# Performance work log

Hardware: AMD Instinct MI355X
Metric: run time of the kernel (lower is better)

The kernel has to match this reference:

```python
import jax, jax.numpy as jnp
import numpy as np

B, S, D = 4, 2048, 1024
NEG = -1e10

def setup_inputs() -> dict:
    key = jax.random.key(0)
    ks = jax.random.split(key, 10)
    inv = 1.0 / np.sqrt(D)
    return {
        "Q": jax.random.normal(ks[0], (B, S, D), dtype=jnp.float32),
        "K": jax.random.normal(ks[1], (B, S, D), dtype=jnp.float32),
        "V": jax.random.normal(ks[2], (B, S, D), dtype=jnp.float32),
        "attention_mask": jax.random.randint(ks[3], (B, 1, S), 0, 2, dtype=jnp.int32),
        "Wq": jax.random.uniform(ks[4], (D, D), jnp.float32, -inv, inv),
        "bq": jnp.zeros((D,), jnp.float32),
        "Wk": jax.random.uniform(ks[5], (D, D), jnp.float32, -inv, inv),
        "bk": jnp.zeros((D,), jnp.float32),
        "Wv": jax.random.uniform(ks[6], (D, D), jnp.float32, -inv, inv),
        "bv": jnp.zeros((D,), jnp.float32),
    }

def reference(Q, K, V, attention_mask, Wq, bq, Wk, bk, Wv, bv):
    # QKV projections (dropout is identity in eval mode)
    q = jnp.einsum('bsd,ed->bse', Q, Wq) + bq  # [B,S,D]
    k = jnp.einsum('bsd,ed->bse', K, Wk) + bk
    v = jnp.einsum('bsd,ed->bse', V, Wv) + bv
    scores = jnp.einsum('bqd,bkd->bqk', q, k) / jnp.sqrt(jnp.float32(D))  # [B,S,S]
    scores = jnp.where(attention_mask == 0, jnp.float32(NEG), scores)
    # additive causal mask: upper triangle (diag=1) gets NEG
    causal = jnp.triu(jnp.full((S, S), NEG, dtype=jnp.float32), k=1)
    scores = scores + causal
    attn = jax.nn.softmax(scores, axis=-1)
    return jnp.einsum('bqk,bkd->bqd', attn, v)
```

## Files before the change

kernel.cpp:

```cpp
#include <hip/hip_runtime.h>
#include <hip/hip_bf16.h>

typedef __bf16 bf16x8 __attribute__((ext_vector_type(8)));
typedef float floatx4 __attribute__((ext_vector_type(4)));
typedef unsigned short ushort_t;

__device__ __forceinline__ bf16x8 load8f(const float* p) {
  const float4* q = reinterpret_cast<const float4*>(p);
  float4 x = q[0], y = q[1];
  bf16x8 r;
  r[0] = (__bf16)x.x; r[1] = (__bf16)x.y; r[2] = (__bf16)x.z; r[3] = (__bf16)x.w;
  r[4] = (__bf16)y.x; r[5] = (__bf16)y.y; r[6] = (__bf16)y.z; r[7] = (__bf16)y.w;
  return r;
}

__device__ __forceinline__ void storeC(float* C, long idx, float v) { C[idx] = v; }
__device__ __forceinline__ void storeC(ushort_t* C, long idx, float v) {
  __bf16 b = (__bf16)v;
  C[idx] = __builtin_bit_cast(ushort_t, b);
}

__device__ __forceinline__ void glds16(const ushort_t* g, ushort_t* l) {
  __builtin_amdgcn_global_load_lds(
      (const __attribute__((address_space(1))) void*)g,
      (__attribute__((address_space(3))) void*)l, 16, 0, 0);
}

__device__ __forceinline__ void bar_raw()  { asm volatile("s_barrier" ::: "memory"); }
__device__ __forceinline__ void lgkm0()    { asm volatile("s_waitcnt lgkmcnt(0)" ::: "memory"); }
__device__ __forceinline__ void wait_vm4() { asm volatile("s_waitcnt vmcnt(4)" ::: "memory"); }
__device__ __forceinline__ void wait_vm0() { asm volatile("s_waitcnt vmcnt(0)" ::: "memory"); }

__global__ __launch_bounds__(256) void cvt3m(
    const float* __restrict__ Q, const float* __restrict__ K,
    const float* __restrict__ V, const float* __restrict__ Wq,
    const float* __restrict__ Wk, const float* __restrict__ Wv,
    ushort_t* __restrict__ dstQ, ushort_t* __restrict__ dstW,
    long nq, long nw,
    const int* __restrict__ mask, int* __restrict__ j0, int S, int B)
{
  const int z = blockIdx.y;
  const long bq = nq >> 11;
  long x = blockIdx.x;
  const float* s; ushort_t* d; long n;
  if (x < bq) {
    s = (z == 0) ? Q : ((z == 1) ? K : V);
    d = dstQ + (long)z * nq; n = nq;
  } else {
    x -= bq;
    s = (z == 0) ? Wq : ((z == 1) ? Wk : Wv);
    d = dstW + (long)z * nw; n = nw;
  }
  const long i = ((x * 256) + threadIdx.x) * 8;
  if (i < n) {
    bf16x8 v = load8f(s + i);
    *reinterpret_cast<bf16x8*>(d + i) = v;
  }
  if (z == 0 && (int)blockIdx.x < B) {
    const int b = blockIdx.x;
    const int* m = mask + (long)b * S;
    const int tid = threadIdx.x;
    int best = S;
    for (int j = tid; j < S; j += 256)
      if (m[j] != 0) best = min(best, j);
    #pragma unroll
    for (int off = 32; off; off >>= 1)
      best = min(best, __shfl_xor(best, off));
    __shared__ int red[4];
    if ((tid & 63) == 0) red[tid >> 6] = best;
    __syncthreads();
    if (tid == 0) j0[b] = min(min(red[0], red[1]), min(red[2], red[3]));
  }
}

template<typename TC>
__device__ __forceinline__ void gemm256_core(
    const ushort_t* __restrict__ Apan,
    const ushort_t* __restrict__ Bpan,
    const float* __restrict__ bias, int bias_mode,
    TC* __restrict__ C, int bm, int bn, int N, int K, int G, float alpha)
{
  __shared__ ushort_t Ab[2][2][128 * 64];
  __shared__ ushort_t Bb[2][2][128 * 64];

  const int tid = threadIdx.x;
  const int wv = tid >> 6;
  const int lane = tid & 63;
  const int wr = wv >> 2, wc = wv & 3;
  const int lr = lane & 15, lq = lane >> 4;

  const int q0 = tid << 4;
  const int r0 = q0 >> 7;
  const int c0 = ((q0 & 127) ^ ((r0 & 7) << 4)) >> 1;
  const int lo0 = q0 >> 1;
  const int lo1 = lo0 + 4096;
  const long Kl = K;

  const ushort_t* As0 = Apan + (long)r0 * Kl + c0;
  const ushort_t* Bs0 = Bpan + (long)r0 * Kl + c0;

  auto stA = [&](int t, int h) {
    const ushort_t* s = As0 + (long)(h * 128) * Kl + t * 64;
    ushort_t* d = &Ab[t & 1][h][0];
    glds16(s, d + lo0);
    glds16(s + 64 * Kl, d + lo1);
  };
  auto stB = [&](int t, int h) {
    const ushort_t* s = Bs0 + (long)(h * 128) * Kl + t * 64;
    ushort_t* d = &Bb[t & 1][h][0];
    glds16(s, d + lo0);
    glds16(s + 64 * Kl, d + lo1);
  };

  const int aco0 = ((lq * 16) ^ ((lr & 7) << 4)) >> 1;
  const int aco1 = ((64 + lq * 16) ^ ((lr & 7) << 4)) >> 1;

  floatx4 acc[8][4];
  #pragma unroll
  for (int i = 0; i < 8; ++i)
    #pragma unroll
    for (int j = 0; j < 4; ++j)
      acc[i][j] = (floatx4){0.f, 0.f, 0.f, 0.f};

  bf16x8 a0[4][2], a1[4][2], b0[2][2], b1[2][2];

  auto ldA4 = [&](bf16x8 (&a)[4][2], int buf, int i0) {
    const ushort_t* Ah = &Ab[buf][wr][lr * 64];
    #pragma unroll
    for (int i = 0; i < 4; ++i) {
      a[i][0] = *reinterpret_cast<const bf16x8*>(Ah + (i0 + i) * 1024 + aco0);
      a[i][1] = *reinterpret_cast<const bf16x8*>(Ah + (i0 + i) * 1024 + aco1);
    }
  };
  auto ldB2 = [&](bf16x8 (&b)[2][2], int buf, int j0) {
    const ushort_t* Bh = &Bb[buf][wc >> 1][(wc & 1) * 4096 + lr * 64];
    #pragma unroll
    for (int j = 0; j < 2; ++j) {
      b[j][0] = *reinterpret_cast<const bf16x8*>(Bh + (j0 + j) * 1024 + aco0);
      b[j][1] = *reinterpret_cast<const bf16x8*>(Bh + (j0 + j) * 1024 + aco1);
    }
  };
  auto MM = [&](int I0, bf16x8 (&AF)[4][2], int J0, bf16x8 (&BF)[2][2]) {
    #pragma unroll
    for (int i = 0; i < 4; ++i)
      #pragma unroll
      for (int j = 0; j < 2; ++j) {
        acc[I0 + i][J0 + j] = __builtin_amdgcn_mfma_f32_16x16x32_bf16(
            AF[i][0], BF[j][0], acc[I0 + i][J0 + j], 0, 0, 0);
        acc[I0 + i][J0 + j] = __builtin_amdgcn_mfma_f32_16x16x32_bf16(
            AF[i][1], BF[j][1], acc[I0 + i][J0 + j], 0, 0, 0);
      }
  };

  stB(0, 0); stB(0, 1);
  stA(0, 0); stA(0, 1);
  stB(1, 0); stB(1, 1);
  wait_vm4();
  bar_raw();

  for (int t = 0; t < G; ++t) {
    const int buf = t & 1;
    ldA4(a0, buf, 0);
    ldB2(b0, buf, 0);
    if (t + 1 < G) stA(t + 1, 0);
    bar_raw(); lgkm0();
    __builtin_amdgcn_s_setprio(1);
    MM(0, a0, 0, b0);
    __builtin_amdgcn_s_setprio(0);
    bar_raw();
    ldB2(b1, buf, 2);
    if (t + 1 < G) stA(t + 1, 1);
    bar_raw(); lgkm0();
    __builtin_amdgcn_s_setprio(1);
    MM(0, a0, 2, b1);
    __builtin_amdgcn_s_setprio(0);
    bar_raw();
    ldA4(a1, buf, 4);
    if (t + 2 < G) stB(t + 2, 0);
    bar_raw(); lgkm0();
    __builtin_amdgcn_s_setprio(1);
    MM(4, a1, 0, b0);
    __builtin_amdgcn_s_setprio(0);
    bar_raw();
    if (t + 2 < G) { stB(t + 2, 1); wait_vm4(); }
    else if (t + 1 < G) wait_vm0();
    bar_raw(); lgkm0();
    __builtin_amdgcn_s_setprio(1);
    MM(4, a1, 2, b1);
    __builtin_amdgcn_s_setprio(0);
    bar_raw();
  }

  #pragma unroll
  for (int i = 0; i < 8; ++i) {
    #pragma unroll
    for (int j = 0; j < 4; ++j) {
      const int row0 = bm * 256 + wr * 128 + i * 16 + lq * 4;
      const int col  = bn * 256 + wc * 64 + j * 16 + lr;
      #pragma unroll
      for (int r = 0; r < 4; ++r) {
        float v = acc[i][j][r] * alpha;
        if (bias_mode == 1) v += bias[col];
        else if (bias_mode == 2) v += bias[row0 + r];
        storeC(C, (long)(row0 + r) * N + col, v);
      }
    }
  }
}

__global__ __launch_bounds__(512) void proj8(
    const ushort_t* __restrict__ Qb, const ushort_t* __restrict__ Wqb,
    const float* __restrict__ bq, const float* __restrict__ bk,
    const float* __restrict__ bv,
    ushort_t* __restrict__ qk, ushort_t* __restrict__ vT,
    long NQ, long NW)
{
  const int h = blockIdx.x;
  const int s = (h & 7) * 48 + (h >> 3);
  int bm, bn, N, mode;
  const ushort_t *A, *Bp;
  ushort_t* Cc;
  const float* bias;
  if (s < 256) {
    const int z = s >> 7, r = s & 127;
    bm = r >> 2; bn = r & 3;
    A  = Qb + (long)z * NQ + (long)bm * 256 * 1024;
    Bp = Wqb + (long)z * NW + (long)bn * 256 * 1024;
    Cc = qk + (long)z * NQ;
    bias = z ? bk : bq; mode = 1; N = 1024;
  } else {
    const int u = s - 256, vb = u >> 5, r = u & 31;
    bm = r >> 3; bn = r & 7;
    A  = Wqb + 2 * NW + (long)bm * 256 * 1024;
    Bp = Qb + 2 * NQ + (long)vb * (2048L * 1024) + (long)bn * 256 * 1024;
    Cc = vT + (long)vb * (1024L * 2048);
    bias = bv; mode = 2; N = 2048;
  }
  gemm256_core<ushort_t>(A, Bp, bias, mode, Cc, bm, bn, N, 1024, 16, 1.0f);
}

__global__ __launch_bounds__(512) void scores8(
    const ushort_t* __restrict__ qb, const ushort_t* __restrict__ kb,
    ushort_t* __restrict__ Sc, const int* __restrict__ j0p)
{
  const int h = blockIdx.x;
  const int job = (h & 7) * 32 + (h >> 3);
  const int bz = job >> 6;
  const int s = job & 63;
  int bm, bn;
  if (s < 36) {
    int r = 0;
    while ((r + 1) * (r + 2) / 2 <= s) ++r;
    bm = r; bn = s - r * (r + 1) / 2;
  } else {
    int u = s - 36, r = 0;
    while (u >= 7 - r) { u -= 7 - r; ++r; }
    bm = r; bn = r + 1 + u;
  }
  if (bn > bm && j0p[bz] <= bm * 256) return;
  const long SD = 2048L * 1024;
  gemm256_core<ushort_t>(qb + (long)bz * SD + (long)bm * 256 * 1024,
                         kb + (long)bz * SD + (long)bn * 256 * 1024,
                         nullptr, 0, Sc + (long)bz * 2048 * 2048,
                         bm, bn, 2048, 1024, 16, 0.03125f);
}

__global__ __launch_bounds__(512) void pv8(
    const ushort_t* __restrict__ P, const ushort_t* __restrict__ vT,
    float* __restrict__ out, float* __restrict__ scr,
    const int* __restrict__ j0p)
{
  const int h = blockIdx.x;
  const int job = (h & 7) * 32 + (h >> 3);
  const int bz = job >> 6;
  const int r = job & 63;
  const int bm = r >> 3;
  const int kh = (r >> 2) & 1;
  const int bn = r & 3;

  const int Gf = (j0p[bz] <= bm * 256) ? (bm + 1) * 4 : 32;
  int g0, g1;
  if (Gf > 8) {
    const int half = Gf >> 1;
    g0 = kh ? half : 0;
    g1 = kh ? Gf : half;
  } else {
    if (kh) return;
    g0 = 0; g1 = Gf;
  }

  float* Cc = kh ? (scr + (long)bz * (2048L * 1024))
                 : (out + (long)bz * (2048L * 1024));
  gemm256_core<float>(
      P  + (long)bz * (2048L * 2048) + (long)bm * 256 * 2048 + g0 * 64,
      vT + (long)bz * (1024L * 2048) + (long)bn * 256 * 2048 + g0 * 64,
      nullptr, 0, Cc, bm, bn, 1024, 2048, g1 - g0, 1.0f);
}

__global__ __launch_bounds__(256) void pv_combine(
    float* __restrict__ out, const float* __restrict__ scr,
    const int* __restrict__ j0p)
{
  const long u = (((long)blockIdx.x * 256) + threadIdx.x) * 8;
  const int bz = (int)(u >> 21);
  const long rem = u & ((1L << 21) - 1);
  const int row = (int)(rem >> 10);
  const int bm = row >> 8;
  const int Gf = (j0p[bz] <= bm * 256) ? (bm + 1) * 4 : 32;
  if (Gf <= 8) return;
  float4* o = reinterpret_cast<float4*>(out + u);
  const float4* s = reinterpret_cast<const float4*>(scr + u);
  float4 o0 = o[0], o1 = o[1], s0 = s[0], s1 = s[1];
  o0.x += s0.x; o0.y += s0.y; o0.z += s0.z; o0.w += s0.w;
  o1.x += s1.x; o1.y += s1.y; o1.z += s1.z; o1.w += s1.w;
  o[0] = o0; o[1] = o1;
}

__global__ __launch_bounds__(256) void softmax_causal(
    const ushort_t* __restrict__ Sc, ushort_t* __restrict__ P,
    const int* __restrict__ mask, const int* __restrict__ j0p, int S)
{
  const int i = blockIdx.x, b = blockIdx.y;
  const ushort_t* row = Sc + ((long)b * S + i) * S;
  ushort_t* prow = P + ((long)b * S + i) * S;
  const int* mrow = mask + (long)b * S;
  const int tid = threadIdx.x;
  const int lane = tid & 63, wave = tid >> 6;
  const int j0 = tid * 8;
  __shared__ float red[4];

  const int blk = i >> 8;
  const int jmax = (j0p[b] <= (blk << 8)) ? ((blk + 1) << 8) : S;
  const bool act = (j0 < jmax);

  float vals[8];
  float mymax = -3.4e38f;
  if (act) {
    bf16x8 sv = *reinterpret_cast<const bf16x8*>(row + j0);
    const int4* mp = reinterpret_cast<const int4*>(mrow + j0);
    int4 m0 = mp[0], m1 = mp[1];
    int mk[8] = {m0.x, m0.y, m0.z, m0.w, m1.x, m1.y, m1.z, m1.w};
    #pragma unroll
    for (int u = 0; u < 8; ++u) {
      const int j = j0 + u;
      float v = (float)sv[u];
      if (mk[u] == 0) v = -1e10f;
      if (j > i) v += -1e10f;
      vals[u] = v;
      mymax = fmaxf(mymax, v);
    }
  }
  #pragma unroll
  for (int off = 32; off; off >>= 1)
    mymax = fmaxf(mymax, __shfl_xor(mymax, off));
  if (lane == 0) red[wave] = mymax;
  __syncthreads();
  const float m = fmaxf(fmaxf(red[0], red[1]), fmaxf(red[2], red[3]));
  __syncthreads();

  float sum = 0.f;
  if (act) {
    #pragma unroll
    for (int u = 0; u < 8; ++u) {
      const float e = __expf(vals[u] - m);
      vals[u] = e;
      sum += e;
    }
  }
  #pragma unroll
  for (int off = 32; off; off >>= 1)
    sum += __shfl_xor(sum, off);
  if (lane == 0) red[wave] = sum;
  __syncthreads();
  const float tot = red[0] + red[1] + red[2] + red[3];
  const float inv = 1.0f / tot;

  if (act) {
    bf16x8 pv;
    #pragma unroll
    for (int u = 0; u < 8; ++u) pv[u] = (__bf16)(vals[u] * inv);
    *reinterpret_cast<bf16x8*>(prow + j0) = pv;
  }
}

extern "C" void kernel_launch(void* const* d_in, const int* in_sizes, int n_in,
                              void* d_out, int out_size, void* d_ws, size_t ws_size,
                              hipStream_t stream)
{
  const int B = 4, S = 2048, D = 1024;
  const float* Q  = (const float*)d_in[0];
  const float* K  = (const float*)d_in[1];
  const float* V  = (const float*)d_in[2];
  const int*   am = (const int*)d_in[3];
  const float* Wq = (const float*)d_in[4];
  const float* bq = (const float*)d_in[5];
  const float* Wk = (const float*)d_in[6];
  const float* bk = (const float*)d_in[7];
  const float* Wv = (const float*)d_in[8];
  const float* bv = (const float*)d_in[9];
  float* out = (float*)d_out;

  const long MS = (long)B * S;
  const long NQ = MS * D;
  const long NW = (long)D * D;

  ushort_t* qb = (ushort_t*)d_ws;
  ushort_t* kb = qb + NQ;
  ushort_t* vT = kb + NQ;
  ushort_t* Qb = vT + NQ;
  ushort_t* Wqb = Qb + 3 * NQ;
  int* j0 = (int*)(Wqb + 3 * NW);
  ushort_t* Sc = Qb;
  ushort_t* P  = qb;
  float* scr   = (float*)Qb;

  cvt3m<<<dim3((int)(NQ / 2048 + NW / 2048), 3), dim3(256), 0, stream>>>(
      Q, K, V, Wq, Wk, Wv, Qb, Wqb, NQ, NW, am, j0, S, B);

  proj8<<<dim3(384), dim3(512), 0, stream>>>(Qb, Wqb, bq, bk, bv, qb, vT, NQ, NW);

  scores8<<<dim3(256), dim3(512), 0, stream>>>(qb, kb, Sc, j0);

  softmax_causal<<<dim3(S, B), dim3(256), 0, stream>>>(Sc, P, am, j0, S);

  pv8<<<dim3(256), dim3(512), 0, stream>>>(P, vT, out, scr, j0);
  pv_combine<<<dim3((int)(MS * D / 8 / 256)), dim3(256), 0, stream>>>(out, scr, j0);
}
```

Baseline: 322.5 us.

## Restructure GEMM main loop to one barrier per tile with staged lgkm waits

Replaces the four-phase inner loop, which had a barrier and a full LDS wait around each MFMA quarter, with a single-phase schedule. All global-to-LDS loads for the next tile are issued up front, all LDS fragment reads for the current tile follow, and each MFMA group waits only on its own reads through partial lgkmcnt counts. One vmcnt(0) and one barrier close each iteration. This is meant to cut barrier and wait overhead and overlap LDS reads with MFMA. In exchange the prefetch distance drops from two B tiles ahead to one tile, and the partial lgkmcnt thresholds have to match the exact number of issued LDS reads.

```diff
diff --git a/kernel.cpp b/kernel.cpp
--- a/kernel.cpp
+++ b/kernel.cpp
@@ -27,9 +27,19 @@
 }
 
 __device__ __forceinline__ void bar_raw()  { asm volatile("s_barrier" ::: "memory"); }
-__device__ __forceinline__ void lgkm0()    { asm volatile("s_waitcnt lgkmcnt(0)" ::: "memory"); }
-__device__ __forceinline__ void wait_vm4() { asm volatile("s_waitcnt vmcnt(4)" ::: "memory"); }
 __device__ __forceinline__ void wait_vm0() { asm volatile("s_waitcnt vmcnt(0)" ::: "memory"); }
+__device__ __forceinline__ void wlg12() {
+  asm volatile("s_waitcnt lgkmcnt(12)" ::: "memory");
+  __builtin_amdgcn_sched_barrier(0);
+}
+__device__ __forceinline__ void wlg8() {
+  asm volatile("s_waitcnt lgkmcnt(8)" ::: "memory");
+  __builtin_amdgcn_sched_barrier(0);
+}
+__device__ __forceinline__ void wlg0() {
+  asm volatile("s_waitcnt lgkmcnt(0)" ::: "memory");
+  __builtin_amdgcn_sched_barrier(0);
+}
 
 __global__ __launch_bounds__(256) void cvt3m(
     const float* __restrict__ Q, const float* __restrict__ K,
@@ -152,42 +162,35 @@
       }
   };
 
-  stB(0, 0); stB(0, 1);
-  stA(0, 0); stA(0, 1);
-  stB(1, 0); stB(1, 1);
-  wait_vm4();
+  stA(0, 0); stA(0, 1); stB(0, 0); stB(0, 1);
+  wait_vm0();
   bar_raw();
 
   for (int t = 0; t < G; ++t) {
     const int buf = t & 1;
+    if (t + 1 < G) { stA(t + 1, 0); stA(t + 1, 1); stB(t + 1, 0); stB(t + 1, 1); }
+    __builtin_amdgcn_sched_barrier(0);
     ldA4(a0, buf, 0);
     ldB2(b0, buf, 0);
-    if (t + 1 < G) stA(t + 1, 0);
-    bar_raw(); lgkm0();
+    __builtin_amdgcn_sched_barrier(0);
+    ldB2(b1, buf, 2);
+    __builtin_amdgcn_sched_barrier(0);
+    ldA4(a1, buf, 4);
+    __builtin_amdgcn_sched_barrier(0);
+    wlg12();
     __builtin_amdgcn_s_setprio(1);
     MM(0, a0, 0, b0);
     __builtin_amdgcn_s_setprio(0);
-    bar_raw();
-    ldB2(b1, buf, 2);
-    if (t + 1 < G) stA(t + 1, 1);
-    bar_raw(); lgkm0();
+    wlg8();
     __builtin_amdgcn_s_setprio(1);
     MM(0, a0, 2, b1);
     __builtin_amdgcn_s_setprio(0);
-    bar_raw();
-    ldA4(a1, buf, 4);
-    if (t + 2 < G) stB(t + 2, 0);
-    bar_raw(); lgkm0();
+    wlg0();
     __builtin_amdgcn_s_setprio(1);
     MM(4, a1, 0, b0);
-    __builtin_amdgcn_s_setprio(0);
-    bar_raw();
-    if (t + 2 < G) { stB(t + 2, 1); wait_vm4(); }
-    else if (t + 1 < G) wait_vm0();
-    bar_raw(); lgkm0();
-    __builtin_amdgcn_s_setprio(1);
     MM(4, a1, 2, b1);
     __builtin_amdgcn_s_setprio(0);
+    wait_vm0();
     bar_raw();
   }
 
```

Measured after the change: 325.3 us. About the same (+0.8%).

## Move V projection into the scores kernel to balance GPU waves

Applied to the files above, without the earlier changes.

Q/K projections now run in their own 256-block launch. The V projection, which was the half-wave tail of the old projection launch, is merged into the scores launch. The scores launch has causal and mask-skipped tiles that exit early, so the V projection GEMM tiles can use the CUs that would otherwise sit idle. This removes a partially filled wave in the projection stage. The cost is a larger, more heterogeneous kernel, which relies on Sc aliasing only the Q/K staging region and not the V input.

```diff
diff --git a/kernel.cpp b/kernel.cpp
--- a/kernel.cpp
+++ b/kernel.cpp
@@ -208,61 +208,58 @@
   }
 }
 
-__global__ __launch_bounds__(512) void proj8(
+__global__ __launch_bounds__(512) void projQK(
     const ushort_t* __restrict__ Qb, const ushort_t* __restrict__ Wqb,
     const float* __restrict__ bq, const float* __restrict__ bk,
+    ushort_t* __restrict__ qk, long NQ, long NW)
+{
+  const int h = blockIdx.x;
+  const int s = (h & 7) * 32 + (h >> 3);
+  const int z = s >> 7, r = s & 127;
+  const int bm = r >> 2, bn = r & 3;
+  gemm256_core<ushort_t>(Qb + (long)z * NQ + (long)bm * 256 * 1024,
+                         Wqb + (long)z * NW + (long)bn * 256 * 1024,
+                         z ? bk : bq, 1, qk + (long)z * NQ,
+                         bm, bn, 1024, 1024, 16, 1.0f);
+}
+
+__global__ __launch_bounds__(512) void sv8(
+    const ushort_t* __restrict__ qb, const ushort_t* __restrict__ kb,
+    const ushort_t* __restrict__ Vb, const ushort_t* __restrict__ Wvb,
     const float* __restrict__ bv,
-    ushort_t* __restrict__ qk, ushort_t* __restrict__ vT,
-    long NQ, long NW)
+    ushort_t* __restrict__ Sc, ushort_t* __restrict__ vT,
+    const int* __restrict__ j0p)
 {
   const int h = blockIdx.x;
   const int s = (h & 7) * 48 + (h >> 3);
-  int bm, bn, N, mode;
-  const ushort_t *A, *Bp;
-  ushort_t* Cc;
-  const float* bias;
-  if (s < 256) {
-    const int z = s >> 7, r = s & 127;
-    bm = r >> 2; bn = r & 3;
-    A  = Qb + (long)z * NQ + (long)bm * 256 * 1024;
-    Bp = Wqb + (long)z * NW + (long)bn * 256 * 1024;
-    Cc = qk + (long)z * NQ;
-    bias = z ? bk : bq; mode = 1; N = 1024;
+  if (s < 128) {
+    const int vb = s >> 5, r = s & 31;
+    const int bm = r >> 3, bn = r & 7;
+    gemm256_core<ushort_t>(Wvb + (long)bm * 256 * 1024,
+                           Vb + (long)vb * (2048L * 1024) + (long)bn * 256 * 1024,
+                           bv, 2, vT + (long)vb * (1024L * 2048),
+                           bm, bn, 2048, 1024, 16, 1.0f);
   } else {
-    const int u = s - 256, vb = u >> 5, r = u & 31;
-    bm = r >> 3; bn = r & 7;
-    A  = Wqb + 2 * NW + (long)bm * 256 * 1024;
-    Bp = Qb + 2 * NQ + (long)vb * (2048L * 1024) + (long)bn * 256 * 1024;
-    Cc = vT + (long)vb * (1024L * 2048);
-    bias = bv; mode = 2; N = 2048;
-  }
-  gemm256_core<ushort_t>(A, Bp, bias, mode, Cc, bm, bn, N, 1024, 16, 1.0f);
-}
-
-__global__ __launch_bounds__(512) void scores8(
-    const ushort_t* __restrict__ qb, const ushort_t* __restrict__ kb,
-    ushort_t* __restrict__ Sc, const int* __restrict__ j0p)
-{
-  const int h = blockIdx.x;
-  const int job = (h & 7) * 32 + (h >> 3);
-  const int bz = job >> 6;
-  const int s = job & 63;
-  int bm, bn;
-  if (s < 36) {
-    int r = 0;
-    while ((r + 1) * (r + 2) / 2 <= s) ++r;
-    bm = r; bn = s - r * (r + 1) / 2;
-  } else {
-    int u = s - 36, r = 0;
-    while (u >= 7 - r) { u -= 7 - r; ++r; }
-    bm = r; bn = r + 1 + u;
-  }
-  if (bn > bm && j0p[bz] <= bm * 256) return;
-  const long SD = 2048L * 1024;
-  gemm256_core<ushort_t>(qb + (long)bz * SD + (long)bm * 256 * 1024,
-                         kb + (long)bz * SD + (long)bn * 256 * 1024,
-                         nullptr, 0, Sc + (long)bz * 2048 * 2048,
-                         bm, bn, 2048, 1024, 16, 0.03125f);
+    const int job = s - 128;
+    const int bz = job >> 6;
+    const int t = job & 63;
+    int bm, bn;
+    if (t < 36) {
+      int r = 0;
+      while ((r + 1) * (r + 2) / 2 <= t) ++r;
+      bm = r; bn = t - r * (r + 1) / 2;
+    } else {
+      int u = t - 36, r = 0;
+      while (u >= 7 - r) { u -= 7 - r; ++r; }
+      bm = r; bn = r + 1 + u;
+    }
+    if (bn > bm && j0p[bz] <= bm * 256) return;
+    const long SD = 2048L * 1024;
+    gemm256_core<ushort_t>(qb + (long)bz * SD + (long)bm * 256 * 1024,
+                           kb + (long)bz * SD + (long)bn * 256 * 1024,
+                           nullptr, 0, Sc + (long)bz * 2048 * 2048,
+                           bm, bn, 2048, 1024, 16, 0.03125f);
+  }
 }
 
 __global__ __launch_bounds__(512) void pv8(
@@ -417,9 +414,10 @@
   cvt3m<<<dim3((int)(NQ / 2048 + NW / 2048), 3), dim3(256), 0, stream>>>(
       Q, K, V, Wq, Wk, Wv, Qb, Wqb, NQ, NW, am, j0, S, B);
 
-  proj8<<<dim3(384), dim3(512), 0, stream>>>(Qb, Wqb, bq, bk, bv, qb, vT, NQ, NW);
-
-  scores8<<<dim3(256), dim3(512), 0, stream>>>(qb, kb, Sc, j0);
+  projQK<<<dim3(256), dim3(512), 0, stream>>>(Qb, Wqb, bq, bk, qb, NQ, NW);
+
+  sv8<<<dim3(384), dim3(512), 0, stream>>>(qb, kb, Qb + 2 * NQ, Wqb + 2 * NW,
+                                           bv, Sc, vT, j0);
 
   softmax_causal<<<dim3(S, B), dim3(256), 0, stream>>>(Sc, P, am, j0, S);
 
```

After: 318.9 us. Within noise of the previous version (-1.1%).
